# Kernel optimization log

Measured on AMD Instinct MI355X. Metric: run time of the kernel, lower is better.

The kernel has to match this reference:

```python
import jax, jax.numpy as jnp
import numpy as np

H = 8    # num_heads (per-head feature size after the quirky split)
D_H = 16 # dim_heads (becomes the effective number of heads after split)


def _split_heads(x, B):
    # torch.split(x, H, dim=-1) then cat on dim 0: new_batch = chunk*B + b
    Bt, T, N, D = x.shape
    dh = D // H
    return x.reshape(B, T, N, dh, H).transpose(3, 0, 1, 2, 4).reshape(dh * B, T, N, H)


def _merge_heads(x, B):
    dhB, T, N, Hh = x.shape
    dh = dhB // B
    return x.reshape(dh, B, T, N, Hh).transpose(1, 2, 3, 0, 4).reshape(B, T, N, dh * Hh)


def setup_inputs() -> dict:
    key = jax.random.key(0)
    ks = jax.random.split(key, 10)
    B, T, N, D = 8, 64, 256, 128
    s_in = 1.0 / np.sqrt(2 * D)
    s_d = 1.0 / np.sqrt(D)
    return {
        "X": jax.random.normal(ks[0], (B, T, N, D), jnp.float32),
        "STE": jax.random.normal(ks[1], (B, T, N, D), jnp.float32),
        "Wq": jax.random.normal(ks[2], (2 * D, D), jnp.float32) * s_in,
        "bq": jnp.zeros((D,), jnp.float32),
        "Wk": jax.random.normal(ks[3], (2 * D, D), jnp.float32) * s_in,
        "bk": jnp.zeros((D,), jnp.float32),
        "Wv": jax.random.normal(ks[4], (2 * D, D), jnp.float32) * s_in,
        "bv": jnp.zeros((D,), jnp.float32),
        "Wo": jax.random.normal(ks[5], (D, D), jnp.float32) * s_d,
        "bo": jnp.zeros((D,), jnp.float32),
    }


def reference(X, STE, Wq, bq, Wk, bk, Wv, bv, Wo, bo):
    B, T, N, D = X.shape
    Xc = jnp.concatenate([X, STE], axis=-1)  # [B,T,N,2D]
    Q = jax.nn.relu(Xc @ Wq + bq)
    K = jax.nn.relu(Xc @ Wk + bk)
    V = jax.nn.relu(Xc @ Wv + bv)
    Q = _split_heads(Q, B)  # [dh*B, T, N, H]
    K = _split_heads(K, B)
    V = _split_heads(V, B)
    # scores over time per vertex: [dh*B, N, T, T]
    scores = jnp.einsum("btnh,bsnh->bnts", Q, K) / jnp.sqrt(jnp.float32(D_H))
    causal = jnp.tril(jnp.ones((T, T), bool))
    scores = jnp.where(causal, scores, -jnp.inf)
    attn = jax.nn.softmax(scores, axis=-1)
    out = jnp.einsum("bnts,bsnh->btnh", attn, V)  # [dh*B, T, N, H]
    out = _merge_heads(out, B)  # [B,T,N,D]
    return jax.nn.relu(out @ Wo + bo)
```

## Files before the change

kernel.cpp:

```cpp
#include <hip/hip_runtime.h>

using bf16x8  = __attribute__((ext_vector_type(8))) __bf16;
using f32x4   = __attribute__((ext_vector_type(4))) float;
using short8  = __attribute__((ext_vector_type(8))) short;
using float4v = __attribute__((ext_vector_type(4))) float;
using uint2v  = __attribute__((ext_vector_type(2))) unsigned int;

#if __has_builtin(__builtin_amdgcn_exp2f)
#define EXP2F(x) __builtin_amdgcn_exp2f(x)
#else
#define EXP2F(x) __expf((x) * 0.6931472f)
#endif
#if __has_builtin(__builtin_amdgcn_rcpf)
#define RCPF(x) __builtin_amdgcn_rcpf(x)
#else
#define RCPF(x) (1.f / (x))
#endif

static __device__ __forceinline__ unsigned short bfu(float f) {
    return __builtin_bit_cast(unsigned short, (__bf16)f);
}
static __device__ __forceinline__ unsigned int pkbf(float a, float b) {
    return (unsigned int)bfu(a) | ((unsigned int)bfu(b) << 16);
}
static __device__ __forceinline__ bf16x8 as_bf(short8 s) {
    return __builtin_bit_cast(bf16x8, s);
}

__global__ void prep_weights(const float* __restrict__ Wq, const float* __restrict__ Wk,
                             const float* __restrict__ Wv, const float* __restrict__ Wo,
                             unsigned short* __restrict__ wq2, unsigned short* __restrict__ wo2) {
    int idx = blockIdx.x * 256 + threadIdx.x;
    if (idx < 384 * 256) {
        int c = idx >> 8, k = idx & 255;
        float v = (c < 128) ? Wq[k * 128 + c]
                : (c < 256) ? Wk[k * 128 + (c - 128)]
                            : Wv[k * 128 + (c - 256)];
        wq2[(k >> 5) * 12288 + (c << 5) + (k & 31)] = bfu(v);
    } else {
        int j = idx - 384 * 256;
        int c = j >> 7, k = j & 127;
        wo2[(k >> 5) * 4096 + (c << 5) + (k & 31)] = bfu(Wo[k * 128 + c]);
    }
}

__global__ __launch_bounds__(256, 2)
void fused_attn(const float* __restrict__ X, const float* __restrict__ STE,
                const float* __restrict__ bq, const float* __restrict__ bk,
                const float* __restrict__ bv, const float* __restrict__ bo,
                const unsigned short* __restrict__ wq2, const unsigned short* __restrict__ wo2,
                float* __restrict__ out) {
    __shared__ __align__(16) char sm[81920];
    constexpr int SXC = 0, SQK = 32768, SV = 65536;
    const float SC2 = 0.36067376f;

    const int tid  = threadIdx.x;
    const int lane = tid & 63;
    const int w    = tid >> 6;
    const int bid  = blockIdx.x;
    const int n    = bid & 255;
    const int b    = bid >> 8;
    const int lr   = lane & 15;
    const int lg   = lane >> 4;
    const int rswA = (lr & 7) << 6;
    const int rswQ = ((lr & 7) << 6) ^ ((lr & 8) << 2);
    const int rswP = (lr & 7) << 4;

    const float* xbase = X   + (size_t)(b * 16384 + n) * 128;
    const float* sbase = STE + (size_t)(b * 16384 + n) * 128;
    #pragma unroll
    for (int it = 0; it < 16; ++it) {
        int t = w + it * 4;
        int j = lane;
        const float* src = (j < 32) ? (xbase + (size_t)t * 32768 + j * 4)
                                    : (sbase + (size_t)t * 32768 + (j - 32) * 4);
        float4v v = *reinterpret_cast<const float4v*>(src);
        uint2v d;
        d[0] = pkbf(v[0], v[1]);
        d[1] = pkbf(v[2], v[3]);
        *reinterpret_cast<uint2v*>(sm + SXC + (t << 9) + ((j * 8) ^ ((t & 7) << 6))) = d;
    }
    __syncthreads();

    const int c0 = w * 96;
    f32x4 acc[4][6];
    #pragma unroll
    for (int m = 0; m < 4; ++m)
        #pragma unroll
        for (int i = 0; i < 6; ++i)
            acc[m][i] = f32x4{0.f, 0.f, 0.f, 0.f};

    bf16x8 bnxt[6];
    #pragma unroll
    for (int i = 0; i < 6; ++i)
        bnxt[i] = as_bf(*reinterpret_cast<const short8*>(
            wq2 + (size_t)(c0 + i * 16 + lr) * 32 + lg * 8));

    #pragma unroll
    for (int ks = 0; ks < 8; ++ks) {
        bf16x8 bcur[6];
        #pragma unroll
        for (int i = 0; i < 6; ++i) bcur[i] = bnxt[i];
        if (ks < 7) {
            #pragma unroll
            for (int i = 0; i < 6; ++i)
                bnxt[i] = as_bf(*reinterpret_cast<const short8*>(
                    wq2 + (size_t)(ks + 1) * 12288 + (size_t)(c0 + i * 16 + lr) * 32 + lg * 8));
        }
        bf16x8 a[4];
        #pragma unroll
        for (int m = 0; m < 4; ++m)
            a[m] = as_bf(*reinterpret_cast<const short8*>(
                sm + SXC + ((m * 16 + lr) << 9) + ((ks * 64 + lg * 16) ^ rswA)));
        #pragma unroll
        for (int m = 0; m < 4; ++m)
            #pragma unroll
            for (int i = 0; i < 6; ++i)
                acc[m][i] = __builtin_amdgcn_mfma_f32_16x16x32_bf16(a[m], bcur[i], acc[m][i], 0, 0, 0);
    }

    #pragma unroll
    for (int i = 0; i < 6; ++i) {
        int c = c0 + i * 16 + lr;
        if (c < 256) {
            float bvv = (c < 128) ? bq[c] : bk[c & 127];
            #pragma unroll
            for (int m = 0; m < 4; ++m)
                #pragma unroll
                for (int r = 0; r < 4; ++r) {
                    int t = m * 16 + lg * 4 + r;
                    *reinterpret_cast<unsigned short*>(
                        sm + SQK + (t << 9) + ((c * 2) ^ (((t & 7) << 6) ^ ((t & 8) << 2))))
                        = bfu(fmaxf(acc[m][i][r] + bvv, 0.f));
                }
        } else {
            int cv = c - 256;
            float bvv = bv[cv];
            #pragma unroll
            for (int m = 0; m < 4; ++m) {
                uint2v d;
                d[0] = pkbf(fmaxf(acc[m][i][0] + bvv, 0.f), fmaxf(acc[m][i][1] + bvv, 0.f));
                d[1] = pkbf(fmaxf(acc[m][i][2] + bvv, 0.f), fmaxf(acc[m][i][3] + bvv, 0.f));
                *reinterpret_cast<uint2v*>(
                    sm + SV + (cv << 7) + ((m * 32 + lg * 8) ^ ((cv & 7) << 4))) = d;
            }
        }
    }
    __syncthreads();

    const f32x4 zf = {0.f, 0.f, 0.f, 0.f};
    const short8 z8 = {0, 0, 0, 0, 0, 0, 0, 0};
    short8 ones8;
    #pragma unroll
    for (int h = 0; h < 8; ++h) ones8[h] = (short)0x3F80;
    char* Pb = sm + SXC + w * 8192;

    #pragma unroll 1
    for (int ci = 0; ci < 4; ++ci) {
        const int cb  = (w * 4 + ci) * 8;
        const int cbB = cb * 2;

        bf16x8 kf[4], qf[4];
        #pragma unroll
        for (int j = 0; j < 4; ++j) {
            kf[j] = (lg == 0)
                ? as_bf(*reinterpret_cast<const short8*>(
                      sm + SQK + ((j * 16 + lr) << 9) + ((256 + cbB) ^ rswQ)))
                : as_bf(z8);
            qf[j] = (lg == 0)
                ? as_bf(*reinterpret_cast<const short8*>(
                      sm + SQK + ((j * 16 + lr) << 9) + (cbB ^ rswQ)))
                : as_bf(z8);
        }

        #pragma unroll
        for (int nt = 0; nt < 4; ++nt) {
            #pragma unroll
            for (int st = 0; st < 4; ++st) {
                if (st > nt) continue;
                f32x4 sv = __builtin_amdgcn_mfma_f32_16x16x32_bf16(kf[st], qf[nt], zf, 0, 0, 0);
                float p[4];
                #pragma unroll
                for (int r = 0; r < 4; ++r) p[r] = EXP2F(sv[r] * SC2);
                if (st == nt) {
                    #pragma unroll
                    for (int r = 0; r < 4; ++r) p[r] = (lg * 4 + r <= lr) ? p[r] : 0.f;
                }
                uint2v d;
                d[0] = pkbf(p[0], p[1]);
                d[1] = pkbf(p[2], p[3]);
                *reinterpret_cast<uint2v*>(
                    Pb + ((nt * 16 + lr) << 7) + ((st * 32 + lg * 8) ^ rswP)) = d;
            }
        }
        {
            uint2v z2; z2[0] = 0; z2[1] = 0;
            *reinterpret_cast<uint2v*>(Pb + (lr << 7) + ((32 + lg * 8) ^ rswP)) = z2;
            *reinterpret_cast<uint2v*>(Pb + ((32 + lr) << 7) + ((96 + lg * 8) ^ rswP)) = z2;
        }
        asm volatile("" ::: "memory");

        f32x4 o[4] = {zf, zf, zf, zf};
        #pragma unroll
        for (int ks = 0; ks < 2; ++ks) {
            int vr = min(cb + lr, 127);
            bf16x8 vf = as_bf(*reinterpret_cast<const short8*>(
                sm + SV + (vr << 7) + ((ks * 64 + lg * 16) ^ ((vr & 7) << 4))));
            if (lr == 8 || lr == 12) vf = as_bf(ones8);
            #pragma unroll
            for (int nt = 0; nt < 4; ++nt) {
                if (nt < 2 * ks) continue;
                bf16x8 pf = as_bf(*reinterpret_cast<const short8*>(
                    Pb + ((nt * 16 + lr) << 7) + ((ks * 64 + lg * 16) ^ rswP)));
                o[nt] = __builtin_amdgcn_mfma_f32_16x16x32_bf16(vf, pf, o[nt], 0, 0, 0);
            }
        }
        asm volatile("" ::: "memory");

        #pragma unroll
        for (int nt = 0; nt < 4; ++nt) {
            float l   = __shfl_xor(o[nt][0], 32);
            float inv = RCPF(l);
            if (lg < 2) {
                int t_ = nt * 16 + lr;
                uint2v d;
                d[0] = pkbf(o[nt][0] * inv, o[nt][1] * inv);
                d[1] = pkbf(o[nt][2] * inv, o[nt][3] * inv);
                *reinterpret_cast<uint2v*>(
                    sm + SQK + (t_ << 9) + ((cbB + lg * 8) ^ rswQ)) = d;
            }
        }
    }
    __syncthreads();

    f32x4 acc2[4][2];
    #pragma unroll
    for (int m = 0; m < 4; ++m)
        #pragma unroll
        for (int i = 0; i < 2; ++i)
            acc2[m][i] = zf;

    #pragma unroll
    for (int ks = 0; ks < 4; ++ks) {
        bf16x8 a2[4];
        #pragma unroll
        for (int m = 0; m < 4; ++m)
            a2[m] = as_bf(*reinterpret_cast<const short8*>(
                sm + SQK + ((m * 16 + lr) << 9) + ((ks * 64 + lg * 16) ^ rswQ)));
        bf16x8 b2[2];
        #pragma unroll
        for (int i = 0; i < 2; ++i)
            b2[i] = as_bf(*reinterpret_cast<const short8*>(
                wo2 + (size_t)ks * 4096 + (size_t)((w + 4 * i) * 16 + lr) * 32 + lg * 8));
        #pragma unroll
        for (int m = 0; m < 4; ++m)
            #pragma unroll
            for (int i = 0; i < 2; ++i)
                acc2[m][i] = __builtin_amdgcn_mfma_f32_16x16x32_bf16(a2[m], b2[i], acc2[m][i], 0, 0, 0);
    }

    float* obase = out + (size_t)(b * 16384 + n) * 128;
    #pragma unroll
    for (int i = 0; i < 2; ++i) {
        int c = (w + 4 * i) * 16 + lr;
        float bias = bo[c];
        #pragma unroll
        for (int m = 0; m < 4; ++m)
            #pragma unroll
            for (int r = 0; r < 4; ++r) {
                int tt = m * 16 + lg * 4 + r;
                obase[(size_t)tt * 32768 + c] = fmaxf(acc2[m][i][r] + bias, 0.f);
            }
    }
}

extern "C" void kernel_launch(void* const* d_in, const int* in_sizes, int n_in,
                              void* d_out, int out_size, void* d_ws, size_t ws_size,
                              hipStream_t stream) {
    const float* X   = (const float*)d_in[0];
    const float* STE = (const float*)d_in[1];
    const float* Wq  = (const float*)d_in[2];
    const float* bq  = (const float*)d_in[3];
    const float* Wk  = (const float*)d_in[4];
    const float* bk  = (const float*)d_in[5];
    const float* Wv  = (const float*)d_in[6];
    const float* bv  = (const float*)d_in[7];
    const float* Wo  = (const float*)d_in[8];
    const float* bo  = (const float*)d_in[9];
    float* out = (float*)d_out;

    unsigned short* wq2 = (unsigned short*)d_ws;
    unsigned short* wo2 = wq2 + 384 * 256;

    prep_weights<<<448, 256, 0, stream>>>(Wq, Wk, Wv, Wo, wq2, wo2);
    fused_attn<<<2048, 256, 0, stream>>>(X, STE, bq, bk, bv, bo, wq2, wo2, out);
}
```

Measured before the change: 90.92 us.

## Shrink LDS to raise occupancy: direct global A loads, register-shuffled P

Removes the LDS staging buffer for the concatenated X/STE input. The first GEMM now loads fp32 rows straight from global memory into MFMA operands and converts them to bf16 in registers. The attention probabilities no longer go through a per-wave LDS scratch; they are passed to the PV MFMA through cross-lane shuffles, and Q/K are split into separate narrower LDS regions. These changes cut shared memory from 80KB to 48KB so launch bounds can target 3 blocks per CU. The costs are uncoalesced strided global reads in the GEMM, the loss of weight-load prefetching, and extra shuffle instructions.

```diff
diff --git a/kernel.cpp b/kernel.cpp
--- a/kernel.cpp
+++ b/kernel.cpp
@@ -25,6 +25,12 @@
 }
 static __device__ __forceinline__ bf16x8 as_bf(short8 s) {
     return __builtin_bit_cast(bf16x8, s);
+}
+static __device__ __forceinline__ bf16x8 cvt8(float4v lo, float4v hi) {
+    union { unsigned int u[4]; bf16x8 v; } r;
+    r.u[0] = pkbf(lo[0], lo[1]); r.u[1] = pkbf(lo[2], lo[3]);
+    r.u[2] = pkbf(hi[0], hi[1]); r.u[3] = pkbf(hi[2], hi[3]);
+    return r.v;
 }
 
 __global__ void prep_weights(const float* __restrict__ Wq, const float* __restrict__ Wk,
@@ -44,14 +50,14 @@
     }
 }
 
-__global__ __launch_bounds__(256, 2)
+__global__ __launch_bounds__(256, 3)
 void fused_attn(const float* __restrict__ X, const float* __restrict__ STE,
                 const float* __restrict__ bq, const float* __restrict__ bk,
                 const float* __restrict__ bv, const float* __restrict__ bo,
                 const unsigned short* __restrict__ wq2, const unsigned short* __restrict__ wo2,
                 float* __restrict__ out) {
-    __shared__ __align__(16) char sm[81920];
-    constexpr int SXC = 0, SQK = 32768, SV = 65536;
+    __shared__ __align__(16) char sm[49152];
+    constexpr int SQ = 0, SK = 16384, SV = 32768;
     const float SC2 = 0.36067376f;
 
     const int tid  = threadIdx.x;
@@ -62,25 +68,17 @@
     const int b    = bid >> 8;
     const int lr   = lane & 15;
     const int lg   = lane >> 4;
-    const int rswA = (lr & 7) << 6;
-    const int rswQ = ((lr & 7) << 6) ^ ((lr & 8) << 2);
-    const int rswP = (lr & 7) << 4;
-
-    const float* xbase = X   + (size_t)(b * 16384 + n) * 128;
-    const float* sbase = STE + (size_t)(b * 16384 + n) * 128;
-    #pragma unroll
-    for (int it = 0; it < 16; ++it) {
-        int t = w + it * 4;
-        int j = lane;
-        const float* src = (j < 32) ? (xbase + (size_t)t * 32768 + j * 4)
-                                    : (sbase + (size_t)t * 32768 + (j - 32) * 4);
-        float4v v = *reinterpret_cast<const float4v*>(src);
-        uint2v d;
-        d[0] = pkbf(v[0], v[1]);
-        d[1] = pkbf(v[2], v[3]);
-        *reinterpret_cast<uint2v*>(sm + SXC + (t << 9) + ((j * 8) ^ ((t & 7) << 6))) = d;
-    }
-    __syncthreads();
+    const int rsw  = (lr & 7) << 4;
+
+    const size_t base = (size_t)(b * 16384 + n) * 128;
+    const float* xr[4];
+    const float* sr[4];
+    #pragma unroll
+    for (int m = 0; m < 4; ++m) {
+        size_t t = m * 16 + lr;
+        xr[m] = X   + base + t * 32768;
+        sr[m] = STE + base + t * 32768;
+    }
 
     const int c0 = w * 96;
     f32x4 acc[4][6];
@@ -90,28 +88,21 @@
         for (int i = 0; i < 6; ++i)
             acc[m][i] = f32x4{0.f, 0.f, 0.f, 0.f};
 
-    bf16x8 bnxt[6];
-    #pragma unroll
-    for (int i = 0; i < 6; ++i)
-        bnxt[i] = as_bf(*reinterpret_cast<const short8*>(
-            wq2 + (size_t)(c0 + i * 16 + lr) * 32 + lg * 8));
-
     #pragma unroll
     for (int ks = 0; ks < 8; ++ks) {
         bf16x8 bcur[6];
         #pragma unroll
-        for (int i = 0; i < 6; ++i) bcur[i] = bnxt[i];
-        if (ks < 7) {
-            #pragma unroll
-            for (int i = 0; i < 6; ++i)
-                bnxt[i] = as_bf(*reinterpret_cast<const short8*>(
-                    wq2 + (size_t)(ks + 1) * 12288 + (size_t)(c0 + i * 16 + lr) * 32 + lg * 8));
-        }
+        for (int i = 0; i < 6; ++i)
+            bcur[i] = as_bf(*reinterpret_cast<const short8*>(
+                wq2 + (size_t)ks * 12288 + (size_t)(c0 + i * 16 + lr) * 32 + lg * 8));
         bf16x8 a[4];
         #pragma unroll
-        for (int m = 0; m < 4; ++m)
-            a[m] = as_bf(*reinterpret_cast<const short8*>(
-                sm + SXC + ((m * 16 + lr) << 9) + ((ks * 64 + lg * 16) ^ rswA)));
+        for (int m = 0; m < 4; ++m) {
+            const float* rp = ((ks < 4) ? xr[m] : sr[m]) + (ks & 3) * 32 + lg * 8;
+            float4v lo = *reinterpret_cast<const float4v*>(rp);
+            float4v hi = *reinterpret_cast<const float4v*>(rp + 4);
+            a[m] = cvt8(lo, hi);
+        }
         #pragma unroll
         for (int m = 0; m < 4; ++m)
             #pragma unroll
@@ -123,14 +114,16 @@
     for (int i = 0; i < 6; ++i) {
         int c = c0 + i * 16 + lr;
         if (c < 256) {
-            float bvv = (c < 128) ? bq[c] : bk[c & 127];
+            int qi = c >> 7, cc = c & 127;
+            char* rbase = sm + (qi ? SK : SQ);
+            float bvv = (qi ? bk : bq)[cc];
             #pragma unroll
             for (int m = 0; m < 4; ++m)
                 #pragma unroll
                 for (int r = 0; r < 4; ++r) {
                     int t = m * 16 + lg * 4 + r;
                     *reinterpret_cast<unsigned short*>(
-                        sm + SQK + (t << 9) + ((c * 2) ^ (((t & 7) << 6) ^ ((t & 8) << 2))))
+                        rbase + (t << 8) + ((cc * 2) ^ ((t & 7) << 4)))
                         = bfu(fmaxf(acc[m][i][r] + bvv, 0.f));
                 }
         } else {
@@ -153,7 +146,6 @@
     short8 ones8;
     #pragma unroll
     for (int h = 0; h < 8; ++h) ones8[h] = (short)0x3F80;
-    char* Pb = sm + SXC + w * 8192;
 
     #pragma unroll 1
     for (int ci = 0; ci < 4; ++ci) {
@@ -165,19 +157,28 @@
         for (int j = 0; j < 4; ++j) {
             kf[j] = (lg == 0)
                 ? as_bf(*reinterpret_cast<const short8*>(
-                      sm + SQK + ((j * 16 + lr) << 9) + ((256 + cbB) ^ rswQ)))
+                      sm + SK + ((j * 16 + lr) << 8) + (cbB ^ rsw)))
                 : as_bf(z8);
             qf[j] = (lg == 0)
                 ? as_bf(*reinterpret_cast<const short8*>(
-                      sm + SQK + ((j * 16 + lr) << 9) + (cbB ^ rswQ)))
+                      sm + SQ + ((j * 16 + lr) << 8) + (cbB ^ rsw)))
                 : as_bf(z8);
         }
+        bf16x8 vf[2];
+        #pragma unroll
+        for (int ks = 0; ks < 2; ++ks) {
+            int vr = min(cb + lr, 127);
+            vf[ks] = as_bf(*reinterpret_cast<const short8*>(
+                sm + SV + (vr << 7) + ((ks * 64 + lg * 16) ^ ((vr & 7) << 4))));
+            if (lr == 8 || lr == 12) vf[ks] = as_bf(ones8);
+        }
 
         #pragma unroll
         for (int nt = 0; nt < 4; ++nt) {
+            unsigned int p2[4][2];
             #pragma unroll
             for (int st = 0; st < 4; ++st) {
-                if (st > nt) continue;
+                if (st > nt) { p2[st][0] = 0; p2[st][1] = 0; continue; }
                 f32x4 sv = __builtin_amdgcn_mfma_f32_16x16x32_bf16(kf[st], qf[nt], zf, 0, 0, 0);
                 float p[4];
                 #pragma unroll
@@ -186,48 +187,35 @@
                     #pragma unroll
                     for (int r = 0; r < 4; ++r) p[r] = (lg * 4 + r <= lr) ? p[r] : 0.f;
                 }
-                uint2v d;
-                d[0] = pkbf(p[0], p[1]);
-                d[1] = pkbf(p[2], p[3]);
-                *reinterpret_cast<uint2v*>(
-                    Pb + ((nt * 16 + lr) << 7) + ((st * 32 + lg * 8) ^ rswP)) = d;
-            }
-        }
-        {
-            uint2v z2; z2[0] = 0; z2[1] = 0;
-            *reinterpret_cast<uint2v*>(Pb + (lr << 7) + ((32 + lg * 8) ^ rswP)) = z2;
-            *reinterpret_cast<uint2v*>(Pb + ((32 + lr) << 7) + ((96 + lg * 8) ^ rswP)) = z2;
-        }
-        asm volatile("" ::: "memory");
-
-        f32x4 o[4] = {zf, zf, zf, zf};
-        #pragma unroll
-        for (int ks = 0; ks < 2; ++ks) {
-            int vr = min(cb + lr, 127);
-            bf16x8 vf = as_bf(*reinterpret_cast<const short8*>(
-                sm + SV + (vr << 7) + ((ks * 64 + lg * 16) ^ ((vr & 7) << 4))));
-            if (lr == 8 || lr == 12) vf = as_bf(ones8);
-            #pragma unroll
-            for (int nt = 0; nt < 4; ++nt) {
+                p2[st][0] = pkbf(p[0], p[1]);
+                p2[st][1] = pkbf(p[2], p[3]);
+            }
+
+            f32x4 o = zf;
+            #pragma unroll
+            for (int ks = 0; ks < 2; ++ks) {
                 if (nt < 2 * ks) continue;
-                bf16x8 pf = as_bf(*reinterpret_cast<const short8*>(
-                    Pb + ((nt * 16 + lr) << 7) + ((ks * 64 + lg * 16) ^ rswP)));
-                o[nt] = __builtin_amdgcn_mfma_f32_16x16x32_bf16(vf, pf, o[nt], 0, 0, 0);
-            }
-        }
-        asm volatile("" ::: "memory");
-
-        #pragma unroll
-        for (int nt = 0; nt < 4; ++nt) {
-            float l   = __shfl_xor(o[nt][0], 32);
+                unsigned int bw[4];
+                #pragma unroll
+                for (int q = 0; q < 4; ++q) {
+                    int srcl = lr + 16 * (2 * (lg & 1) + (q >> 1));
+                    unsigned int v0 = __shfl(p2[2 * ks][q & 1], srcl);
+                    unsigned int v1 = __shfl(p2[2 * ks + 1][q & 1], srcl);
+                    bw[q] = (lg & 2) ? v1 : v0;
+                }
+                bf16x8 pf = __builtin_bit_cast(bf16x8, bw);
+                o = __builtin_amdgcn_mfma_f32_16x16x32_bf16(vf[ks], pf, o, 0, 0, 0);
+            }
+
+            float l   = __shfl_xor(o[0], 32);
             float inv = RCPF(l);
             if (lg < 2) {
                 int t_ = nt * 16 + lr;
                 uint2v d;
-                d[0] = pkbf(o[nt][0] * inv, o[nt][1] * inv);
-                d[1] = pkbf(o[nt][2] * inv, o[nt][3] * inv);
+                d[0] = pkbf(o[0] * inv, o[1] * inv);
+                d[1] = pkbf(o[2] * inv, o[3] * inv);
                 *reinterpret_cast<uint2v*>(
-                    sm + SQK + (t_ << 9) + ((cbB + lg * 8) ^ rswQ)) = d;
+                    sm + SQ + (t_ << 8) + ((cbB + lg * 8) ^ rsw)) = d;
             }
         }
     }
@@ -246,7 +234,7 @@
         #pragma unroll
         for (int m = 0; m < 4; ++m)
             a2[m] = as_bf(*reinterpret_cast<const short8*>(
-                sm + SQK + ((m * 16 + lr) << 9) + ((ks * 64 + lg * 16) ^ rswQ)));
+                sm + SQ + ((m * 16 + lr) << 8) + ((ks * 64 + lg * 16) ^ rsw)));
         bf16x8 b2[2];
         #pragma unroll
         for (int i = 0; i < 2; ++i)
@@ -259,7 +247,7 @@
                 acc2[m][i] = __builtin_amdgcn_mfma_f32_16x16x32_bf16(a2[m], b2[i], acc2[m][i], 0, 0, 0);
     }
 
-    float* obase = out + (size_t)(b * 16384 + n) * 128;
+    float* obase = out + base;
     #pragma unroll
     for (int i = 0; i < 2; ++i) {
         int c = (w + 4 * i) * 16 + lr;
```

New measurement: 137.2 us. +50.9%, slower.
